# Performance work log

Hardware: AMD Instinct MI355X
Metric: run time of the kernel (lower is better)

Reference implementation:

```python
import jax, jax.numpy as jnp
import numpy as np

B, T, C = 8, 2048, 1024
CONTEXT_SIZE = T  # repo ties context_size to sequence length of the mask


def setup_inputs() -> dict:
    key = jax.random.key(0)
    ks = jax.random.split(key, 7)
    s = 1.0 / np.sqrt(C)
    return {
        "x": jax.random.normal(ks[0], (B, T, C), dtype=jnp.float32),
        "Wq": jax.random.normal(ks[1], (C, C), dtype=jnp.float32) * s,
        "bq": jax.random.normal(ks[2], (C,), dtype=jnp.float32) * s,
        "Wk": jax.random.normal(ks[3], (C, C), dtype=jnp.float32) * s,
        "bk": jax.random.normal(ks[4], (C,), dtype=jnp.float32) * s,
        "Wv": jax.random.normal(ks[5], (C, C), dtype=jnp.float32) * s,
        "bv": jax.random.normal(ks[6], (C,), dtype=jnp.float32) * s,
    }


def reference(x, Wq, bq, Wk, bk, Wv, bv):
    # x: [B, T, C]; weights stored as [in, out] so y = x @ W + b (same math as nn.Linear)
    Tlen = x.shape[1]
    q = x @ Wq + bq
    k = x @ Wk + bk
    v = x @ Wv + bv
    # NOTE: original scales by context_size**-0.5 (seq-length based), not head-dim
    scale = jnp.asarray(CONTEXT_SIZE, x.dtype) ** -0.5
    scores = jnp.einsum("btc,bsc->bts", q, k) * scale  # [B, T, T]
    causal = jnp.tril(jnp.ones((Tlen, Tlen), dtype=bool))
    scores = jnp.where(causal, scores, -jnp.inf)
    attn = jax.nn.softmax(scores, axis=-1)
    return jnp.einsum("bts,bsc->btc", attn, v)
```

## Files before the change

### kernel.cpp

```cpp
#include <hip/hip_runtime.h>

#define B_SZ 8
#define T_SZ 2048
#define C_SZ 1024

typedef __attribute__((ext_vector_type(8))) short short8;
typedef __attribute__((ext_vector_type(8))) unsigned short ushort8;
typedef __attribute__((ext_vector_type(16))) float f32x16;

__device__ __forceinline__ unsigned short f2bf(float x) {
  union { float f; unsigned u; } v; v.f = x;
  unsigned r = v.u + 0x7FFFu + ((v.u >> 16) & 1u);
  return (unsigned short)(r >> 16);
}
__device__ __forceinline__ float bf2f(unsigned short h) {
  union { unsigned u; float f; } v; v.u = ((unsigned)h) << 16;
  return v.f;
}

__device__ __forceinline__ void gload16(const void* g, void* l) {
  __builtin_amdgcn_global_load_lds(
      (const __attribute__((address_space(1))) unsigned int*)(uintptr_t)g,
      (__attribute__((address_space(3))) unsigned int*)(uintptr_t)l, 16, 0, 0);
}

__device__ __forceinline__ int xcd_swz(int orig, int nwg) {
  const int q = nwg >> 3, r = nwg & 7;
  const int xcd = orig & 7, off = orig >> 3;
  return (xcd < r ? xcd * (q + 1) : r * (q + 1) + (xcd - r) * q) + off;
}

#define WAITV(N) asm volatile("s_waitcnt vmcnt(" #N ")" ::: "memory")
#define BARRIER_()                 \
  do {                             \
    __builtin_amdgcn_s_barrier();  \
    asm volatile("" ::: "memory"); \
  } while (0)

template <int LDA, int LDB>
__device__ __forceinline__ void nt8_core(const unsigned short* __restrict__ Ab,
                                         const unsigned short* __restrict__ Bb,
                                         const int NT, unsigned short* lds,
                                         f32x16 (&acc)[4][2]) {
  const int lane = threadIdx.x & 63;
  const int wid = threadIdx.x >> 6;
  const int wr = wid >> 2;
  const int wc = wid & 3;

  const int srow = lane >> 2;
  const int sswz = ((lane & 3) ^ (srow & 3)) * 8;
  const unsigned short* gA0 = Ab + (size_t)(wid * 16 + srow) * LDA + sswz;
  const unsigned short* gA1 = gA0 + (size_t)128 * LDA;
  const unsigned short* gB0 = Bb + (size_t)(wid * 16 + srow) * LDB + sswz;
  const unsigned short* gB1 = gB0 + (size_t)128 * LDB;

  const int arow = (wr * 128 + (lane & 31)) * 32;
  const int brow = (wc * 64 + (lane & 31)) * 32 + 8192;
  const int sw0 = (((lane >> 5) ^ (lane & 3)) * 8);
  const int sw1 = (((2 + (lane >> 5)) ^ (lane & 3)) * 8);

#define GSTAGE(tt, ss)                                                        \
  {                                                                           \
    gload16(gA0 + (size_t)(tt) * 32, lds + (ss) * 16384 + wid * 512);         \
    gload16(gA1 + (size_t)(tt) * 32, lds + (ss) * 16384 + 4096 + wid * 512);  \
    gload16(gB0 + (size_t)(tt) * 32, lds + (ss) * 16384 + 8192 + wid * 512);  \
    gload16(gB1 + (size_t)(tt) * 32, lds + (ss) * 16384 + 12288 + wid * 512); \
  }

#define COMPUTE(U)                                                             \
  {                                                                            \
    short8 af[4][2], bg[2][2];                                                 \
    _Pragma("unroll") for (int mb = 0; mb < 4; ++mb) {                         \
      af[mb][0] =                                                              \
          *(const short8*)(lds + (U) * 16384 + arow + mb * 1024 + sw0);        \
      af[mb][1] =                                                              \
          *(const short8*)(lds + (U) * 16384 + arow + mb * 1024 + sw1);        \
    }                                                                          \
    _Pragma("unroll") for (int nb = 0; nb < 2; ++nb) {                         \
      bg[nb][0] =                                                              \
          *(const short8*)(lds + (U) * 16384 + brow + nb * 1024 + sw0);        \
      bg[nb][1] =                                                              \
          *(const short8*)(lds + (U) * 16384 + brow + nb * 1024 + sw1);        \
    }                                                                          \
    __builtin_amdgcn_s_setprio(1);                                             \
    _Pragma("unroll") for (int ks = 0; ks < 2; ++ks)                           \
        _Pragma("unroll") for (int mb = 0; mb < 4; ++mb)                       \
            _Pragma("unroll") for (int nb = 0; nb < 2; ++nb) acc[mb][nb] =     \
        __builtin_amdgcn_mfma_f32_32x32x16_bf16(af[mb][ks], bg[nb][ks],        \
                                                acc[mb][nb], 0, 0, 0);         \
    __builtin_amdgcn_s_setprio(0);                                             \
  }

  GSTAGE(0, 0);
  GSTAGE(1, 1);
  GSTAGE(2, 2);
  WAITV(8);
  BARRIER_();

  int tb = 0;
  for (; tb + 8 <= NT; tb += 4) {
    GSTAGE(tb + 3, 3); COMPUTE(0); WAITV(8); BARRIER_();
    GSTAGE(tb + 4, 0); COMPUTE(1); WAITV(8); BARRIER_();
    GSTAGE(tb + 5, 1); COMPUTE(2); WAITV(8); BARRIER_();
    GSTAGE(tb + 6, 2); COMPUTE(3); WAITV(8); BARRIER_();
  }
  GSTAGE(tb + 3, 3); COMPUTE(0); WAITV(8); BARRIER_();
  COMPUTE(1); WAITV(4); BARRIER_();
  COMPUTE(2); WAITV(0); BARRIER_();
  COMPUTE(3);
#undef GSTAGE
#undef COMPUTE
}

__global__ __launch_bounds__(256) void convert_x(const float* __restrict__ x,
                                                 unsigned short* __restrict__ Xb,
                                                 int n8) {
  for (int i = blockIdx.x * blockDim.x + threadIdx.x; i < n8;
       i += gridDim.x * blockDim.x) {
    const float4* p = (const float4*)(x + (size_t)i * 8);
    float4 a = p[0], b = p[1];
    ushort8 u;
    u[0] = f2bf(a.x); u[1] = f2bf(a.y); u[2] = f2bf(a.z); u[3] = f2bf(a.w);
    u[4] = f2bf(b.x); u[5] = f2bf(b.y); u[6] = f2bf(b.z); u[7] = f2bf(b.w);
    *(ushort8*)(Xb + (size_t)i * 8) = u;
  }
}

__global__ __launch_bounds__(256) void transpose_w(
    const float* __restrict__ Wq, const float* __restrict__ Wk,
    const float* __restrict__ Wv, unsigned short* __restrict__ Wt) {
  const int z = blockIdx.z;
  const float* W = z == 0 ? Wq : (z == 1 ? Wk : Wv);
  unsigned short* O = Wt + (size_t)z * C_SZ * C_SZ;
  __shared__ float tl[32][33];
  const int bx = blockIdx.x * 32;
  const int by = blockIdx.y * 32;
  const int tx = threadIdx.x & 31;
  const int ty = threadIdx.x >> 5;
#pragma unroll
  for (int j = 0; j < 4; ++j)
    tl[ty + j * 8][tx] = W[(size_t)(by + ty + j * 8) * C_SZ + bx + tx];
  __syncthreads();
#pragma unroll
  for (int j = 0; j < 4; ++j)
    O[(size_t)(bx + ty + j * 8) * C_SZ + by + tx] = f2bf(tl[tx][ty + j * 8]);
}

__global__ __launch_bounds__(256) void transpose_v(
    const unsigned short* __restrict__ V, unsigned short* __restrict__ Vt) {
  const int b = blockIdx.z;
  __shared__ unsigned short tl[64][66];
  const int bx = blockIdx.x * 64;
  const int by = blockIdx.y * 64;
  const int tx = threadIdx.x & 63;
  const int ty = threadIdx.x >> 6;
  const unsigned short* Vb = V + (size_t)b * T_SZ * C_SZ;
  unsigned short* Ob = Vt + (size_t)b * C_SZ * T_SZ;
#pragma unroll
  for (int r = 0; r < 16; ++r)
    tl[ty * 16 + r][tx] = Vb[(size_t)(by + ty * 16 + r) * C_SZ + bx + tx];
  __syncthreads();
#pragma unroll
  for (int r = 0; r < 16; ++r)
    Ob[(size_t)(bx + ty * 16 + r) * T_SZ + by + tx] = tl[tx][ty * 16 + r];
}

__global__ __launch_bounds__(512, 2) void qkv_fused(
    const unsigned short* __restrict__ Xb, const unsigned short* __restrict__ Wt,
    const float* __restrict__ bq, const float* __restrict__ bk,
    const float* __restrict__ bv, unsigned short* __restrict__ QKV) {
  __shared__ unsigned short lds[65536] __attribute__((aligned(16)));
  const int wg = xcd_swz(blockIdx.x, 3 * 64 * 4);
  const int z = wg >> 8;
  const int rem = wg & 255;
  const int m0 = (rem >> 2) * 256;
  const int n0 = (rem & 3) * 256;
  const float* bias = z == 0 ? bq : (z == 1 ? bk : bv);

  f32x16 acc[4][2] = {};
  nt8_core<C_SZ, C_SZ>(Xb + (size_t)m0 * C_SZ,
                       Wt + (size_t)z * C_SZ * C_SZ + (size_t)n0 * C_SZ,
                       C_SZ / 32, lds, acc);

  unsigned short* Y = QKV + (size_t)z * B_SZ * T_SZ * C_SZ;
  const int lane = threadIdx.x & 63;
  const int wid = threadIdx.x >> 6;
  const int wr = wid >> 2, wc = wid & 3;
#pragma unroll
  for (int nb = 0; nb < 2; ++nb) {
    const int col = n0 + wc * 64 + nb * 32 + (lane & 31);
    const float bvv = bias[col];
#pragma unroll
    for (int mb = 0; mb < 4; ++mb) {
      const int rbase = m0 + wr * 128 + mb * 32 + 4 * (lane >> 5);
#pragma unroll
      for (int r = 0; r < 16; ++r) {
        const int row = rbase + (r & 3) + 8 * (r >> 2);
        Y[(size_t)row * C_SZ + col] = f2bf(acc[mb][nb][r] + bvv);
      }
    }
  }
}

__global__ __launch_bounds__(512, 2) void scores_gemm(
    const unsigned short* __restrict__ Q, const unsigned short* __restrict__ Km,
    unsigned short* __restrict__ S, float scale) {
  const int wg = xcd_swz(blockIdx.x, B_SZ * 8 * 8);
  const int b = wg >> 6;
  const int rem = wg & 63;
  const int mt = rem >> 3, nt = rem & 7;
  if (nt > mt) return;
  const int m0 = mt * 256, n0 = nt * 256;
  __shared__ unsigned short lds[65536] __attribute__((aligned(16)));

  f32x16 acc[4][2] = {};
  nt8_core<C_SZ, C_SZ>(Q + (size_t)b * T_SZ * C_SZ + (size_t)m0 * C_SZ,
                       Km + (size_t)b * T_SZ * C_SZ + (size_t)n0 * C_SZ,
                       C_SZ / 32, lds, acc);

  unsigned short* Sb = S + (size_t)b * T_SZ * T_SZ;
  const int lane = threadIdx.x & 63;
  const int wid = threadIdx.x >> 6;
  const int wr = wid >> 2, wc = wid & 3;
#pragma unroll
  for (int nb = 0; nb < 2; ++nb) {
    const int col = n0 + wc * 64 + nb * 32 + (lane & 31);
#pragma unroll
    for (int mb = 0; mb < 4; ++mb) {
      const int rbase = m0 + wr * 128 + mb * 32 + 4 * (lane >> 5);
#pragma unroll
      for (int r = 0; r < 16; ++r) {
        const int row = rbase + (r & 3) + 8 * (r >> 2);
        Sb[(size_t)row * T_SZ + col] = f2bf(acc[mb][nb][r] * scale);
      }
    }
  }
}

__device__ __forceinline__ float wredmax(float v) {
#pragma unroll
  for (int o = 32; o > 0; o >>= 1) v = fmaxf(v, __shfl_xor(v, o, 64));
  return v;
}
__device__ __forceinline__ float wredsum(float v) {
#pragma unroll
  for (int o = 32; o > 0; o >>= 1) v += __shfl_xor(v, o, 64);
  return v;
}

__global__ __launch_bounds__(256) void softmax_causal(
    unsigned short* __restrict__ S) {
  const int row = blockIdx.x;
  const int b = row >> 11;
  const int tq = row & (T_SZ - 1);
  unsigned short* sr = S + (size_t)b * T_SZ * T_SZ + (size_t)tq * T_SZ;
  const int len = tq + 1;
  const int wlen = (len + 255) & ~255;
  const int tid = threadIdx.x;
  const int lane = tid & 63;
  const int wid = tid >> 6;
  const int i0 = tid * 8;
  __shared__ float red[4];

  const ushort8 raw = *(const ushort8*)(sr + i0);
  float v[8];
  float mx = -1e30f;
#pragma unroll
  for (int j = 0; j < 8; ++j) {
    v[j] = (i0 + j < len) ? bf2f(raw[j]) : -1e30f;
    mx = fmaxf(mx, v[j]);
  }
  mx = wredmax(mx);
  if (lane == 0) red[wid] = mx;
  __syncthreads();
  mx = fmaxf(fmaxf(red[0], red[1]), fmaxf(red[2], red[3]));
  __syncthreads();

  float sm = 0.f;
#pragma unroll
  for (int j = 0; j < 8; ++j) {
    v[j] = __expf(v[j] - mx);
    sm += v[j];
  }
  sm = wredsum(sm);
  if (lane == 0) red[wid] = sm;
  __syncthreads();
  sm = red[0] + red[1] + red[2] + red[3];
  const float inv = 1.f / sm;

  if (i0 < wlen) {
    ushort8 o;
#pragma unroll
    for (int j = 0; j < 8; ++j)
      o[j] = (i0 + j < len) ? f2bf(v[j] * inv) : (unsigned short)0;
    *(ushort8*)(sr + i0) = o;
  }
}

__global__ __launch_bounds__(512, 2) void pv_gemm(
    const unsigned short* __restrict__ P, const unsigned short* __restrict__ Vt,
    float* __restrict__ O) {
  const int wg = xcd_swz(blockIdx.x, B_SZ * 8 * 4);
  const int b = wg >> 5;
  const int rem = wg & 31;
  const int mt = rem >> 2, nt = rem & 3;
  const int m0 = mt * 256, n0 = nt * 256;
  __shared__ unsigned short lds[65536] __attribute__((aligned(16)));

  f32x16 acc[4][2] = {};
  nt8_core<T_SZ, T_SZ>(P + (size_t)b * T_SZ * T_SZ + (size_t)m0 * T_SZ,
                       Vt + (size_t)b * C_SZ * T_SZ + (size_t)n0 * T_SZ,
                       (mt + 1) * 8, lds, acc);

  float* Ob = O + (size_t)b * T_SZ * C_SZ;
  const int lane = threadIdx.x & 63;
  const int wid = threadIdx.x >> 6;
  const int wr = wid >> 2, wc = wid & 3;
#pragma unroll
  for (int nb = 0; nb < 2; ++nb) {
    const int col = n0 + wc * 64 + nb * 32 + (lane & 31);
#pragma unroll
    for (int mb = 0; mb < 4; ++mb) {
      const int rbase = m0 + wr * 128 + mb * 32 + 4 * (lane >> 5);
#pragma unroll
      for (int r = 0; r < 16; ++r) {
        const int row = rbase + (r & 3) + 8 * (r >> 2);
        Ob[(size_t)row * C_SZ + col] = acc[mb][nb][r];
      }
    }
  }
}

extern "C" void kernel_launch(void* const* d_in, const int* in_sizes, int n_in,
                              void* d_out, int out_size, void* d_ws,
                              size_t ws_size, hipStream_t stream) {
  (void)in_sizes; (void)n_in; (void)out_size; (void)ws_size;
  const float* x = (const float*)d_in[0];
  const float* Wq = (const float*)d_in[1];
  const float* bq = (const float*)d_in[2];
  const float* Wk = (const float*)d_in[3];
  const float* bk = (const float*)d_in[4];
  const float* Wv = (const float*)d_in[5];
  const float* bv = (const float*)d_in[6];
  float* out = (float*)d_out;

  const size_t TC = (size_t)B_SZ * T_SZ * C_SZ;
  unsigned short* Q = (unsigned short*)d_ws;
  unsigned short* K = Q + TC;
  unsigned short* V = K + TC;
  unsigned short* S = V + TC;
  unsigned short* Xb = S;
  unsigned short* Wt = S + TC;
  unsigned short* Vt = Q;

  const float scale = 0.022097086912079608f;

  hipLaunchKernelGGL(convert_x, dim3(2048), dim3(256), 0, stream, x, Xb,
                     (int)(TC / 8));
  hipLaunchKernelGGL(transpose_w, dim3(32, 32, 3), dim3(256), 0, stream, Wq,
                     Wk, Wv, Wt);
  hipLaunchKernelGGL(qkv_fused, dim3(3 * 64 * 4), dim3(512), 0, stream, Xb, Wt,
                     bq, bk, bv, Q);
  hipLaunchKernelGGL(scores_gemm, dim3(B_SZ * 8 * 8), dim3(512), 0, stream, Q,
                     K, S, scale);
  hipLaunchKernelGGL(transpose_v, dim3(16, 32, 8), dim3(256), 0, stream, V,
                     Vt);
  hipLaunchKernelGGL(softmax_causal, dim3(B_SZ * T_SZ), dim3(256), 0, stream,
                     S);
  hipLaunchKernelGGL(pv_gemm, dim3(B_SZ * 8 * 4), dim3(512), 0, stream, S, Vt,
                     out);
}
```

Measured before the change: 319.2 us.

## Rewrite GEMM core as 8-wave ping-pong pipeline with 16x16x32 MFMA and K=64 tiles

Replaces the shared GEMM mainloop with a two-buffer, K=64 tile schedule split into half-tile phases. Each phase interleaves LDS fragment reads, async global-to-LDS loads and MFMA bursts between barriers. The change also moves from 32x32x16 to 16x16x32 bf16 MFMA with a new swizzled LDS layout, and drops occupancy to one workgroup per CU. The XCD swizzle is simplified to assume the workgroup count divides by 8. The aim is better overlap of memory and matrix work, at the cost of more barriers and lower occupancy.

```diff
diff --git a/kernel.cpp b/kernel.cpp
--- a/kernel.cpp
+++ b/kernel.cpp
@@ -6,7 +6,7 @@
 
 typedef __attribute__((ext_vector_type(8))) short short8;
 typedef __attribute__((ext_vector_type(8))) unsigned short ushort8;
-typedef __attribute__((ext_vector_type(16))) float f32x16;
+typedef __attribute__((ext_vector_type(4))) float f32x4;
 
 __device__ __forceinline__ unsigned short f2bf(float x) {
   union { float f; unsigned u; } v; v.f = x;
@@ -25,91 +25,116 @@
 }
 
 __device__ __forceinline__ int xcd_swz(int orig, int nwg) {
-  const int q = nwg >> 3, r = nwg & 7;
-  const int xcd = orig & 7, off = orig >> 3;
-  return (xcd < r ? xcd * (q + 1) : r * (q + 1) + (xcd - r) * q) + off;
+  return (orig & 7) * (nwg >> 3) + (orig >> 3);
 }
 
 #define WAITV(N) asm volatile("s_waitcnt vmcnt(" #N ")" ::: "memory")
-#define BARRIER_()                 \
-  do {                             \
-    __builtin_amdgcn_s_barrier();  \
-    asm volatile("" ::: "memory"); \
-  } while (0)
+#define BAR1                            \
+  {                                     \
+    asm volatile("" ::: "memory");      \
+    __builtin_amdgcn_s_barrier();       \
+    __builtin_amdgcn_sched_barrier(0);  \
+    asm volatile("" ::: "memory");      \
+  }
+#define BAR2                            \
+  {                                     \
+    asm volatile("" ::: "memory");      \
+    __builtin_amdgcn_s_barrier();       \
+    asm volatile("" ::: "memory");      \
+  }
 
 template <int LDA, int LDB>
-__device__ __forceinline__ void nt8_core(const unsigned short* __restrict__ Ab,
-                                         const unsigned short* __restrict__ Bb,
-                                         const int NT, unsigned short* lds,
-                                         f32x16 (&acc)[4][2]) {
+__device__ __forceinline__ void nt8p(const unsigned short* __restrict__ Ab,
+                                     const unsigned short* __restrict__ Bb,
+                                     const int NT, unsigned short* lds,
+                                     f32x4 (&acc)[2][4][4]) {
   const int lane = threadIdx.x & 63;
   const int wid = threadIdx.x >> 6;
   const int wr = wid >> 2;
   const int wc = wid & 3;
-
-  const int srow = lane >> 2;
-  const int sswz = ((lane & 3) ^ (srow & 3)) * 8;
-  const unsigned short* gA0 = Ab + (size_t)(wid * 16 + srow) * LDA + sswz;
-  const unsigned short* gA1 = gA0 + (size_t)128 * LDA;
-  const unsigned short* gB0 = Bb + (size_t)(wid * 16 + srow) * LDB + sswz;
-  const unsigned short* gB1 = gB0 + (size_t)128 * LDB;
-
-  const int arow = (wr * 128 + (lane & 31)) * 32;
-  const int brow = (wc * 64 + (lane & 31)) * 32 + 8192;
-  const int sw0 = (((lane >> 5) ^ (lane & 3)) * 8);
-  const int sw1 = (((2 + (lane >> 5)) ^ (lane & 3)) * 8);
-
-#define GSTAGE(tt, ss)                                                        \
-  {                                                                           \
-    gload16(gA0 + (size_t)(tt) * 32, lds + (ss) * 16384 + wid * 512);         \
-    gload16(gA1 + (size_t)(tt) * 32, lds + (ss) * 16384 + 4096 + wid * 512);  \
-    gload16(gB0 + (size_t)(tt) * 32, lds + (ss) * 16384 + 8192 + wid * 512);  \
-    gload16(gB1 + (size_t)(tt) * 32, lds + (ss) * 16384 + 12288 + wid * 512); \
-  }
-
-#define COMPUTE(U)                                                             \
-  {                                                                            \
-    short8 af[4][2], bg[2][2];                                                 \
-    _Pragma("unroll") for (int mb = 0; mb < 4; ++mb) {                         \
-      af[mb][0] =                                                              \
-          *(const short8*)(lds + (U) * 16384 + arow + mb * 1024 + sw0);        \
-      af[mb][1] =                                                              \
-          *(const short8*)(lds + (U) * 16384 + arow + mb * 1024 + sw1);        \
-    }                                                                          \
-    _Pragma("unroll") for (int nb = 0; nb < 2; ++nb) {                         \
-      bg[nb][0] =                                                              \
-          *(const short8*)(lds + (U) * 16384 + brow + nb * 1024 + sw0);        \
-      bg[nb][1] =                                                              \
-          *(const short8*)(lds + (U) * 16384 + brow + nb * 1024 + sw1);        \
-    }                                                                          \
-    __builtin_amdgcn_s_setprio(1);                                             \
-    _Pragma("unroll") for (int ks = 0; ks < 2; ++ks)                           \
-        _Pragma("unroll") for (int mb = 0; mb < 4; ++mb)                       \
-            _Pragma("unroll") for (int nb = 0; nb < 2; ++nb) acc[mb][nb] =     \
-        __builtin_amdgcn_mfma_f32_32x32x16_bf16(af[mb][ks], bg[nb][ks],        \
-                                                acc[mb][nb], 0, 0, 0);         \
-    __builtin_amdgcn_s_setprio(0);                                             \
-  }
-
-  GSTAGE(0, 0);
-  GSTAGE(1, 1);
-  GSTAGE(2, 2);
+  const int fr = lane & 15;
+  const int fq = lane >> 4;
+
+  const int aslot = ((lane & 7) ^ (lane >> 3)) * 8;
+  const int rr0 = (wid * 2 + 0) * 8 + (lane >> 3);
+  const int rr1 = (wid * 2 + 1) * 8 + (lane >> 3);
+  const unsigned short* pA0 =
+      Ab + (size_t)((rr0 >> 6) * 128 + (rr0 & 63)) * LDA + aslot;
+  const unsigned short* pA1 =
+      Ab + (size_t)((rr1 >> 6) * 128 + (rr1 & 63)) * LDA + aslot;
+  const int bslot = ((lane & 3) ^ ((lane >> 3) & 3)) * 8;
+  const unsigned short* pB0 =
+      Bb + (size_t)((wid * 2 + 0) * 16 + (lane >> 2)) * LDB + bslot;
+  const unsigned short* pB1 =
+      Bb + (size_t)((wid * 2 + 1) * 16 + (lane >> 2)) * LDB + bslot;
+  const int ldsC0 = (wid * 2 + 0) * 512;
+  const int ldsC1 = (wid * 2 + 1) * 512;
+
+  const int arb = wr * 4096 + fr * 64;
+  const int asw0 = ((0 * 4 + fq) ^ (fr & 7)) * 8;
+  const int asw1 = ((1 * 4 + fq) ^ (fr & 7)) * 8;
+  const int brb =
+      16384 + (wc * 64 + fr) * 32 + ((fq ^ ((fr >> 1) & 3)) * 8);
+
+#define STG_A(d, h, kt)                                           \
+  {                                                               \
+    gload16(pA0 + (size_t)(h) * 64 * LDA + (size_t)(kt) * 64,     \
+            lds + (d) * 32768 + (h) * 8192 + ldsC0);              \
+    gload16(pA1 + (size_t)(h) * 64 * LDA + (size_t)(kt) * 64,     \
+            lds + (d) * 32768 + (h) * 8192 + ldsC1);              \
+  }
+#define STG_B(d, kh, kt)                                          \
+  {                                                               \
+    gload16(pB0 + (kh) * 32 + (size_t)(kt) * 64,                  \
+            lds + (d) * 32768 + 16384 + (kh) * 8192 + ldsC0);     \
+    gload16(pB1 + (kh) * 32 + (size_t)(kt) * 64,                  \
+            lds + (d) * 32768 + 16384 + (kh) * 8192 + ldsC1);     \
+  }
+#define LDAF(d, r, s)                                             \
+  _Pragma("unroll") for (int mb = 0; mb < 4; ++mb) af[mb] =       \
+      *(const short8*)&lds[(d) * 32768 + (r) * 8192 + arb +       \
+                           mb * 1024 + ((s) ? asw1 : asw0)];
+#define LDBF(d, s)                                                \
+  _Pragma("unroll") for (int nb = 0; nb < 4; ++nb) bf[nb] =       \
+      *(const short8*)&lds[(d) * 32768 + (s) * 8192 + brb + nb * 512];
+#define MM(r)                                                     \
+  __builtin_amdgcn_s_setprio(1);                                  \
+  _Pragma("unroll") for (int mb = 0; mb < 4; ++mb)                \
+  _Pragma("unroll") for (int nb = 0; nb < 4; ++nb)                \
+  acc[r][mb][nb] = __builtin_amdgcn_mfma_f32_16x16x32_bf16(       \
+      af[mb], bf[nb], acc[r][mb][nb], 0, 0, 0);                   \
+  __builtin_amdgcn_s_setprio(0);
+#define TILE_STEP(d, dn, TT)                                                 \
+  {                                                                          \
+    const int tp1 = ((TT) + 1 < NT) ? (TT) + 1 : NT - 1;                     \
+    const int tp2 = ((TT) + 2 < NT) ? (TT) + 2 : NT - 1;                     \
+    short8 af[4], bf[4];                                                     \
+    LDAF(d, 0, 0); LDBF(d, 0); STG_B(dn, 1, tp1); BAR1; MM(0); WAITV(6); BAR2; \
+    LDAF(d, 1, 0); STG_A(dn, 1, tp1); BAR1; MM(1); BAR2;                     \
+    LDAF(d, 0, 1); LDBF(d, 1); STG_B(d, 0, tp2); BAR1; MM(0); BAR2;          \
+    LDAF(d, 1, 1); STG_A(d, 0, tp2); BAR1; MM(1); WAITV(8); BAR2;            \
+  }
+
+  const int t1 = (NT > 1) ? 1 : 0;
+  STG_B(0, 0, 0);
+  STG_A(0, 0, 0);
+  STG_B(0, 1, 0);
+  STG_A(0, 1, 0);
+  STG_B(1, 0, t1);
+  STG_A(1, 0, t1);
   WAITV(8);
-  BARRIER_();
-
-  int tb = 0;
-  for (; tb + 8 <= NT; tb += 4) {
-    GSTAGE(tb + 3, 3); COMPUTE(0); WAITV(8); BARRIER_();
-    GSTAGE(tb + 4, 0); COMPUTE(1); WAITV(8); BARRIER_();
-    GSTAGE(tb + 5, 1); COMPUTE(2); WAITV(8); BARRIER_();
-    GSTAGE(tb + 6, 2); COMPUTE(3); WAITV(8); BARRIER_();
-  }
-  GSTAGE(tb + 3, 3); COMPUTE(0); WAITV(8); BARRIER_();
-  COMPUTE(1); WAITV(4); BARRIER_();
-  COMPUTE(2); WAITV(0); BARRIER_();
-  COMPUTE(3);
-#undef GSTAGE
-#undef COMPUTE
+  BAR2;
+
+  for (int T = 0; T < NT; T += 2) {
+    TILE_STEP(0, 1, T);
+    TILE_STEP(1, 0, T + 1);
+  }
+#undef STG_A
+#undef STG_B
+#undef LDAF
+#undef LDBF
+#undef MM
+#undef TILE_STEP
 }
 
 __global__ __launch_bounds__(256) void convert_x(const float* __restrict__ x,
@@ -165,11 +190,11 @@
     Ob[(size_t)(bx + ty * 16 + r) * T_SZ + by + tx] = tl[tx][ty * 16 + r];
 }
 
-__global__ __launch_bounds__(512, 2) void qkv_fused(
+__global__ __launch_bounds__(512, 1) void qkv_fused(
     const unsigned short* __restrict__ Xb, const unsigned short* __restrict__ Wt,
     const float* __restrict__ bq, const float* __restrict__ bk,
     const float* __restrict__ bv, unsigned short* __restrict__ QKV) {
-  __shared__ unsigned short lds[65536] __attribute__((aligned(16)));
+  __shared__ unsigned short lds[65536] __attribute__((aligned(128)));
   const int wg = xcd_swz(blockIdx.x, 3 * 64 * 4);
   const int z = wg >> 8;
   const int rem = wg & 255;
@@ -177,32 +202,33 @@
   const int n0 = (rem & 3) * 256;
   const float* bias = z == 0 ? bq : (z == 1 ? bk : bv);
 
-  f32x16 acc[4][2] = {};
-  nt8_core<C_SZ, C_SZ>(Xb + (size_t)m0 * C_SZ,
-                       Wt + (size_t)z * C_SZ * C_SZ + (size_t)n0 * C_SZ,
-                       C_SZ / 32, lds, acc);
+  f32x4 acc[2][4][4] = {};
+  nt8p<C_SZ, C_SZ>(Xb + (size_t)m0 * C_SZ,
+                   Wt + (size_t)z * C_SZ * C_SZ + (size_t)n0 * C_SZ,
+                   C_SZ / 64, lds, acc);
 
   unsigned short* Y = QKV + (size_t)z * B_SZ * T_SZ * C_SZ;
   const int lane = threadIdx.x & 63;
   const int wid = threadIdx.x >> 6;
   const int wr = wid >> 2, wc = wid & 3;
-#pragma unroll
-  for (int nb = 0; nb < 2; ++nb) {
-    const int col = n0 + wc * 64 + nb * 32 + (lane & 31);
-    const float bvv = bias[col];
-#pragma unroll
-    for (int mb = 0; mb < 4; ++mb) {
-      const int rbase = m0 + wr * 128 + mb * 32 + 4 * (lane >> 5);
-#pragma unroll
-      for (int r = 0; r < 16; ++r) {
-        const int row = rbase + (r & 3) + 8 * (r >> 2);
-        Y[(size_t)row * C_SZ + col] = f2bf(acc[mb][nb][r] + bvv);
+  const int fr = lane & 15, fq = lane >> 4;
+#pragma unroll
+  for (int r = 0; r < 2; ++r)
+#pragma unroll
+    for (int nb = 0; nb < 4; ++nb) {
+      const int col = n0 + wc * 64 + nb * 16 + fr;
+      const float bvv = bias[col];
+#pragma unroll
+      for (int mb = 0; mb < 4; ++mb) {
+        const int row0 = m0 + wr * 128 + r * 64 + mb * 16 + fq * 4;
+#pragma unroll
+        for (int j = 0; j < 4; ++j)
+          Y[(size_t)(row0 + j) * C_SZ + col] = f2bf(acc[r][mb][nb][j] + bvv);
       }
     }
-  }
-}
-
-__global__ __launch_bounds__(512, 2) void scores_gemm(
+}
+
+__global__ __launch_bounds__(512, 1) void scores_gemm(
     const unsigned short* __restrict__ Q, const unsigned short* __restrict__ Km,
     unsigned short* __restrict__ S, float scale) {
   const int wg = xcd_swz(blockIdx.x, B_SZ * 8 * 8);
@@ -211,30 +237,31 @@
   const int mt = rem >> 3, nt = rem & 7;
   if (nt > mt) return;
   const int m0 = mt * 256, n0 = nt * 256;
-  __shared__ unsigned short lds[65536] __attribute__((aligned(16)));
-
-  f32x16 acc[4][2] = {};
-  nt8_core<C_SZ, C_SZ>(Q + (size_t)b * T_SZ * C_SZ + (size_t)m0 * C_SZ,
-                       Km + (size_t)b * T_SZ * C_SZ + (size_t)n0 * C_SZ,
-                       C_SZ / 32, lds, acc);
+  __shared__ unsigned short lds[65536] __attribute__((aligned(128)));
+
+  f32x4 acc[2][4][4] = {};
+  nt8p<C_SZ, C_SZ>(Q + (size_t)b * T_SZ * C_SZ + (size_t)m0 * C_SZ,
+                   Km + (size_t)b * T_SZ * C_SZ + (size_t)n0 * C_SZ,
+                   C_SZ / 64, lds, acc);
 
   unsigned short* Sb = S + (size_t)b * T_SZ * T_SZ;
   const int lane = threadIdx.x & 63;
   const int wid = threadIdx.x >> 6;
   const int wr = wid >> 2, wc = wid & 3;
-#pragma unroll
-  for (int nb = 0; nb < 2; ++nb) {
-    const int col = n0 + wc * 64 + nb * 32 + (lane & 31);
-#pragma unroll
-    for (int mb = 0; mb < 4; ++mb) {
-      const int rbase = m0 + wr * 128 + mb * 32 + 4 * (lane >> 5);
-#pragma unroll
-      for (int r = 0; r < 16; ++r) {
-        const int row = rbase + (r & 3) + 8 * (r >> 2);
-        Sb[(size_t)row * T_SZ + col] = f2bf(acc[mb][nb][r] * scale);
+  const int fr = lane & 15, fq = lane >> 4;
+#pragma unroll
+  for (int r = 0; r < 2; ++r)
+#pragma unroll
+    for (int nb = 0; nb < 4; ++nb) {
+      const int col = n0 + wc * 64 + nb * 16 + fr;
+#pragma unroll
+      for (int mb = 0; mb < 4; ++mb) {
+        const int row0 = m0 + wr * 128 + r * 64 + mb * 16 + fq * 4;
+#pragma unroll
+        for (int j = 0; j < 4; ++j)
+          Sb[(size_t)(row0 + j) * T_SZ + col] = f2bf(acc[r][mb][nb][j] * scale);
       }
     }
-  }
 }
 
 __device__ __forceinline__ float wredmax(float v) {
@@ -297,7 +324,7 @@
   }
 }
 
-__global__ __launch_bounds__(512, 2) void pv_gemm(
+__global__ __launch_bounds__(512, 1) void pv_gemm(
     const unsigned short* __restrict__ P, const unsigned short* __restrict__ Vt,
     float* __restrict__ O) {
   const int wg = xcd_swz(blockIdx.x, B_SZ * 8 * 4);
@@ -305,30 +332,31 @@
   const int rem = wg & 31;
   const int mt = rem >> 2, nt = rem & 3;
   const int m0 = mt * 256, n0 = nt * 256;
-  __shared__ unsigned short lds[65536] __attribute__((aligned(16)));
-
-  f32x16 acc[4][2] = {};
-  nt8_core<T_SZ, T_SZ>(P + (size_t)b * T_SZ * T_SZ + (size_t)m0 * T_SZ,
-                       Vt + (size_t)b * C_SZ * T_SZ + (size_t)n0 * T_SZ,
-                       (mt + 1) * 8, lds, acc);
+  __shared__ unsigned short lds[65536] __attribute__((aligned(128)));
+
+  f32x4 acc[2][4][4] = {};
+  nt8p<T_SZ, T_SZ>(P + (size_t)b * T_SZ * T_SZ + (size_t)m0 * T_SZ,
+                   Vt + (size_t)b * C_SZ * T_SZ + (size_t)n0 * T_SZ,
+                   4 * (mt + 1), lds, acc);
 
   float* Ob = O + (size_t)b * T_SZ * C_SZ;
   const int lane = threadIdx.x & 63;
   const int wid = threadIdx.x >> 6;
   const int wr = wid >> 2, wc = wid & 3;
-#pragma unroll
-  for (int nb = 0; nb < 2; ++nb) {
-    const int col = n0 + wc * 64 + nb * 32 + (lane & 31);
-#pragma unroll
-    for (int mb = 0; mb < 4; ++mb) {
-      const int rbase = m0 + wr * 128 + mb * 32 + 4 * (lane >> 5);
-#pragma unroll
-      for (int r = 0; r < 16; ++r) {
-        const int row = rbase + (r & 3) + 8 * (r >> 2);
-        Ob[(size_t)row * C_SZ + col] = acc[mb][nb][r];
+  const int fr = lane & 15, fq = lane >> 4;
+#pragma unroll
+  for (int r = 0; r < 2; ++r)
+#pragma unroll
+    for (int nb = 0; nb < 4; ++nb) {
+      const int col = n0 + wc * 64 + nb * 16 + fr;
+#pragma unroll
+      for (int mb = 0; mb < 4; ++mb) {
+        const int row0 = m0 + wr * 128 + r * 64 + mb * 16 + fq * 4;
+#pragma unroll
+        for (int j = 0; j < 4; ++j)
+          Ob[(size_t)(row0 + j) * C_SZ + col] = acc[r][mb][nb][j];
       }
     }
-  }
 }
 
 extern "C" void kernel_launch(void* const* d_in, const int* in_sizes, int n_in,
```

After: 268.8 us. 15.8% less time.
